# Kernel optimization log

Hardware: AMD Instinct MI355X
Metric: run time of the kernel (lower is better)

Reference implementation:

```python
import jax, jax.numpy as jnp
import numpy as np

N_NODES = 100000

def _sage_conv(x, edge_index, W_l, W_r, b):
    # PyG SAGEConv (aggr='mean'): out = lin_l(mean_{j in N(i)} x_j) + lin_r(x_i)
    src, dst = edge_index[0], edge_index[1]
    n = x.shape[0]
    agg = jax.ops.segment_sum(x[src], dst, num_segments=n)        # [N, F]
    deg = jax.ops.segment_sum(jnp.ones((src.shape[0],), x.dtype), dst, num_segments=n)
    mean = agg / jnp.maximum(deg, 1.0)[:, None]
    return mean @ W_l + b + x @ W_r

def setup_inputs() -> dict:
    key = jax.random.key(0)
    ks = jax.random.split(key, 8)
    d_in, d_hid, n_cls, n_edges = 64, 128, 40, 1000000
    x = jax.random.normal(ks[0], (N_NODES, d_in), dtype=jnp.float32)
    edge_index = jax.random.randint(ks[1], (2, n_edges), 0, N_NODES, dtype=jnp.int64)
    W1_l = jax.random.normal(ks[2], (d_in, d_hid), dtype=jnp.float32) * (1.0 / np.sqrt(d_in))
    W1_r = jax.random.normal(ks[3], (d_in, d_hid), dtype=jnp.float32) * (1.0 / np.sqrt(d_in))
    b1 = jnp.zeros((d_hid,), dtype=jnp.float32)
    W2_l = jax.random.normal(ks[4], (d_hid, n_cls), dtype=jnp.float32) * (1.0 / np.sqrt(d_hid))
    W2_r = jax.random.normal(ks[5], (d_hid, n_cls), dtype=jnp.float32) * (1.0 / np.sqrt(d_hid))
    b2 = jnp.zeros((n_cls,), dtype=jnp.float32)
    return {"x": x, "edge_index": edge_index, "W1_l": W1_l, "W1_r": W1_r, "b1": b1,
            "W2_l": W2_l, "W2_r": W2_r, "b2": b2}

def reference(x, edge_index, W1_l, W1_r, b1, W2_l, W2_r, b2):
    h = _sage_conv(x, edge_index, W1_l, W1_r, b1)
    h = jax.nn.relu(h)
    h = _sage_conv(h, edge_index, W2_l, W2_r, b2)
    return jax.nn.log_softmax(h, axis=1)
```

## Files before the change

kernel.cpp:

```cpp
#include <hip/hip_runtime.h>

#define N_NODES 100000
#define N_EDGES 1000000
#define D_IN    64
#define D_HID   128
#define N_CLS   40
#define PAD     48
#define NBUK    391
#define EB      512
#define EPB     1954
#define NCB     6250

typedef float f32x4 __attribute__((ext_vector_type(4)));
typedef float f32x2 __attribute__((ext_vector_type(2)));
typedef short s8v   __attribute__((ext_vector_type(8)));
typedef unsigned short us8 __attribute__((ext_vector_type(8)));

__device__ __forceinline__ unsigned short f2bf(float f) {
    unsigned int b = __float_as_uint(f);
    return (unsigned short)((b + 0x7FFFu + ((b >> 16) & 1u)) >> 16);
}
__device__ __forceinline__ float bf2f(unsigned short u) {
    return __uint_as_float(((unsigned int)u) << 16);
}

#if __has_builtin(__builtin_amdgcn_cvt_pk_f32_fp8) && __has_builtin(__builtin_amdgcn_cvt_pk_fp8_f32)
#define HWFP8 1
#else
#define HWFP8 0
#endif

__device__ __forceinline__ unsigned int f2fp8_sw(float f) {
    const unsigned int b = __float_as_uint(f);
    const float g = __uint_as_float(b & 0x7FFFFFFFu) * 0x1p-120f;
    const unsigned int gb = __float_as_uint(g);
    const unsigned int r = gb + 0x7FFFFu + ((gb >> 20) & 1u);
    return ((b >> 31) << 7) | ((r >> 20) & 0x7Fu);
}
__device__ __forceinline__ float fp82f_sw(unsigned int u) {
    const unsigned int bits = ((u & 0x80u) << 24) | ((u & 0x7Fu) << 20);
    return __uint_as_float(bits) * 0x1p120f;
}
__device__ __forceinline__ unsigned int enc4(float a, float b, float c, float d) {
#if HWFP8
    int v = __builtin_amdgcn_cvt_pk_fp8_f32(a, b, 0, false);
    v = __builtin_amdgcn_cvt_pk_fp8_f32(c, d, v, true);
    return (unsigned int)v;
#else
    return f2fp8_sw(a) | (f2fp8_sw(b) << 8) | (f2fp8_sw(c) << 16) | (f2fp8_sw(d) << 24);
#endif
}
__device__ __forceinline__ void dec8_acc2(uint2 u, f32x2* a2) {
#if HWFP8
    a2[0] += __builtin_amdgcn_cvt_pk_f32_fp8((int)u.x, false);
    a2[1] += __builtin_amdgcn_cvt_pk_f32_fp8((int)u.x, true);
    a2[2] += __builtin_amdgcn_cvt_pk_f32_fp8((int)u.y, false);
    a2[3] += __builtin_amdgcn_cvt_pk_f32_fp8((int)u.y, true);
#else
    a2[0][0] += fp82f_sw(u.x & 0xFFu);        a2[0][1] += fp82f_sw((u.x >> 8) & 0xFFu);
    a2[1][0] += fp82f_sw((u.x >> 16) & 0xFFu); a2[1][1] += fp82f_sw((u.x >> 24) & 0xFFu);
    a2[2][0] += fp82f_sw(u.y & 0xFFu);        a2[2][1] += fp82f_sw((u.y >> 8) & 0xFFu);
    a2[3][0] += fp82f_sw((u.y >> 16) & 0xFFu); a2[3][1] += fp82f_sw((u.y >> 24) & 0xFFu);
#endif
}

__global__ __launch_bounds__(256) void passA_kern(
    const int* __restrict__ dst, int* __restrict__ cnt,
    const float* __restrict__ x,
    unsigned short* __restrict__ xb, unsigned char* __restrict__ xq,
    const float* __restrict__ W1l, const float* __restrict__ W1r,
    const float* __restrict__ W2l, const float* __restrict__ W2r,
    unsigned short* __restrict__ w1f, unsigned short* __restrict__ w2f)
{
    __shared__ int lbuk[NBUK];
    const int t = threadIdx.x;
    const int bid = blockIdx.x;
    if (bid < EB) {
        for (int j = t; j < NBUK; j += 256) lbuk[j] = 0;
        __syncthreads();
        const int e0 = bid * EPB;
        const int e1 = min(e0 + EPB, N_EDGES);
        for (int e = e0 + t; e < e1; e += 256) atomicAdd(&lbuk[dst[e] >> 8], 1);
        __syncthreads();
        for (int j = t; j < NBUK; j += 256) cnt[j * EB + bid] = lbuk[j];
        return;
    }
    const int i = (bid - EB) * 256 + t;
    if (i < 2048) {
        const int fid = i >> 6, l = i & 63;
        const int ct = fid >> 2, ks = fid & 3;
        const int c = ct * 16 + (l & 15);
        const int k0 = ks * 32 + 8 * (l >> 4);
        unsigned short tmp[8];
        #pragma unroll
        for (int j = 0; j < 8; ++j) {
            const int k = k0 + j;
            const float v = (k < 64) ? W1l[k * D_HID + c] : W1r[(k - 64) * D_HID + c];
            tmp[j] = f2bf(v);
        }
        *(s8v*)(w1f + (size_t)fid * 512 + l * 8) = *(s8v*)tmp;
    } else if (i < 2048 + 1280) {
        const int t2 = i - 2048;
        const int fid = t2 >> 6, l = t2 & 63;
        const int c2t = fid >> 2, ks = fid & 3;
        const int c2 = c2t * 16 + (l & 15);
        const int k0 = ks * 32 + 8 * (l >> 4);
        unsigned short tmp[8];
        #pragma unroll
        for (int j = 0; j < 8; ++j) {
            const int k = k0 + j;
            const float v = (c2 < N_CLS) ? W2l[k * N_CLS + c2] : W2r[k * N_CLS + (c2 - N_CLS)];
            tmp[j] = f2bf(v);
        }
        *(s8v*)(w2f + (size_t)fid * 512 + l * 8) = *(s8v*)tmp;
    }
    if (i >= N_NODES * (D_IN / 4)) return;
    const float4 v = reinterpret_cast<const float4*>(x)[i];
    ushort4 o;
    o.x = f2bf(v.x); o.y = f2bf(v.y); o.z = f2bf(v.z); o.w = f2bf(v.w);
    reinterpret_cast<ushort4*>(xb)[i] = o;
    reinterpret_cast<unsigned int*>(xq)[i] = enc4(v.x, v.y, v.z, v.w);
}

__global__ __launch_bounds__(512) void scanS1_kern(int* __restrict__ cnt, int* __restrict__ buktot)
{
    __shared__ int wsum[8];
    __shared__ int woff[8];
    const int buk = blockIdx.x;
    const int t = threadIdx.x;
    const int lane = t & 63, wid = t >> 6;
    const int v = cnt[buk * EB + t];
    int vs = v;
    #pragma unroll
    for (int off = 1; off < 64; off <<= 1) {
        int tt = __shfl_up(vs, off);
        if (lane >= off) vs += tt;
    }
    if (lane == 63) wsum[wid] = vs;
    __syncthreads();
    if (wid == 0 && lane < 8) {
        int w = wsum[lane];
        int ws_ = w;
        #pragma unroll
        for (int off = 1; off < 8; off <<= 1) {
            int tt = __shfl_up(ws_, off);
            if (lane >= off) ws_ += tt;
        }
        woff[lane] = ws_ - w;
        if (lane == 7) buktot[buk] = ws_;
    }
    __syncthreads();
    cnt[buk * EB + t] = woff[wid] + vs - v;
}

__global__ __launch_bounds__(512) void scanS2_kern(const int* __restrict__ buktot, int* __restrict__ bukbase)
{
    __shared__ int wsum[8];
    __shared__ int woff[8];
    const int t = threadIdx.x;
    const int lane = t & 63, wid = t >> 6;
    const int v = (t < NBUK) ? buktot[t] : 0;
    int vs = v;
    #pragma unroll
    for (int off = 1; off < 64; off <<= 1) {
        int tt = __shfl_up(vs, off);
        if (lane >= off) vs += tt;
    }
    if (lane == 63) wsum[wid] = vs;
    __syncthreads();
    if (wid == 0 && lane < 8) {
        int w = wsum[lane];
        int ws_ = w;
        #pragma unroll
        for (int off = 1; off < 8; off <<= 1) {
            int tt = __shfl_up(ws_, off);
            if (lane >= off) ws_ += tt;
        }
        woff[lane] = ws_ - w;
    }
    __syncthreads();
    if (t < NBUK) bukbase[t] = woff[wid] + vs - v;
}

__global__ __launch_bounds__(256) void passA2_kern(
    const int* __restrict__ src, const int* __restrict__ dst,
    const int* __restrict__ cnt, const int* __restrict__ bukbase,
    unsigned int* __restrict__ ebuf)
{
    __shared__ int cur[NBUK];
    const int t = threadIdx.x;
    const int blk = blockIdx.x;
    for (int j = t; j < NBUK; j += 256) cur[j] = bukbase[j] + cnt[j * EB + blk];
    __syncthreads();
    const int e0 = blk * EPB;
    const int e1 = min(e0 + EPB, N_EDGES);
    for (int e = e0 + t; e < e1; e += 256) {
        const int d = dst[e];
        const int slot = atomicAdd(&cur[d >> 8], 1);
        ebuf[slot] = (unsigned int)src[e] | ((unsigned int)(d & 255) << 17);
    }
}

__global__ __launch_bounds__(256) void passB_kern(
    const unsigned int* __restrict__ ebuf,
    const int* __restrict__ bukbase, const int* __restrict__ buktot,
    int* __restrict__ padcsr, int* __restrict__ deg)
{
    __shared__ int lh[256];
    const int t = threadIdx.x;
    const int b = blockIdx.x;
    lh[t] = 0;
    __syncthreads();
    const int base = bukbase[b];
    const int n = buktot[b];
    for (int j = t; j < n; j += 256) {
        const unsigned int u = ebuf[base + j];
        const int dl = (int)(u >> 17);
        const int sr = (int)(u & 0x1FFFFu);
        const int r = atomicAdd(&lh[dl], 1);
        if (r < PAD) padcsr[((b << 8) | dl) * PAD + r] = sr;
    }
    __syncthreads();
    const int node = (b << 8) + t;
    if (node < N_NODES) deg[node] = lh[t];
}

#define MLD 72
__global__ __launch_bounds__(512) void fused_mfma_kern(
    const unsigned short* __restrict__ xb, const unsigned char* __restrict__ xq,
    const int* __restrict__ deg, const int* __restrict__ padcsr,
    const unsigned short* __restrict__ w1f, const unsigned short* __restrict__ w2f,
    const float* __restrict__ b1, const float* __restrict__ b2,
    unsigned char* __restrict__ y2q, unsigned short* __restrict__ yrb)
{
    __shared__ unsigned short hT[8192];
    __shared__ unsigned short mean_lds[64 * MLD];
    const int t = threadIdx.x;
    const int l = t & 63, w = t >> 6;

    {
        const int s = l >> 3, c8 = l & 7;
        const int nl = w * 8 + s;
        const int gnode = blockIdx.x * 64 + nl;
        f32x2 a2[4] = {}, b2v[4] = {};
        float a[8];
        if (gnode < N_NODES) {
            const int dg = deg[gnode];
            const int beg = gnode * PAD;
            const int end = beg + min(dg, PAD);
            int j = beg;
            for (; j + 4 <= end; j += 4) {
                const int s0 = padcsr[j], s1 = padcsr[j + 1], s2 = padcsr[j + 2], s3 = padcsr[j + 3];
                const uint2 u0 = *(const uint2*)(xq + (size_t)s0 * D_IN + c8 * 8);
                const uint2 u1 = *(const uint2*)(xq + (size_t)s1 * D_IN + c8 * 8);
                const uint2 u2 = *(const uint2*)(xq + (size_t)s2 * D_IN + c8 * 8);
                const uint2 u3 = *(const uint2*)(xq + (size_t)s3 * D_IN + c8 * 8);
                dec8_acc2(u0, a2); dec8_acc2(u1, b2v);
                dec8_acc2(u2, a2); dec8_acc2(u3, b2v);
            }
            for (; j < end; ++j) {
                const int s0 = padcsr[j];
                const uint2 u0 = *(const uint2*)(xq + (size_t)s0 * D_IN + c8 * 8);
                dec8_acc2(u0, a2);
            }
            const float invd = 1.0f / fmaxf((float)dg, 1.0f);
            #pragma unroll
            for (int i = 0; i < 4; ++i) {
                a2[i] += b2v[i];
                a[2 * i]     = a2[i][0] * invd;
                a[2 * i + 1] = a2[i][1] * invd;
            }
        } else {
            #pragma unroll
            for (int i = 0; i < 8; ++i) a[i] = 0.f;
        }
        us8 o;
        #pragma unroll
        for (int i = 0; i < 8; ++i) o[i] = f2bf(a[i]);
        *(us8*)(mean_lds + nl * MLD + c8 * 8) = o;
    }
    __syncthreads();

    const int nt = w & 3;
    const int cg = w >> 2;
    const int node = blockIdx.x * 64 + nt * 16 + (l & 15);
    const int kc = 8 * (l >> 4);

    const unsigned short* xrow = xb + (size_t)node * D_IN;
    const unsigned short* mbase = mean_lds + (nt * 16 + (l & 15)) * MLD;
    s8v bfr[4];
    bfr[0] = *(const s8v*)(mbase + kc);
    bfr[1] = *(const s8v*)(mbase + 32 + kc);
    bfr[2] = *(const s8v*)(xrow + kc);
    bfr[3] = *(const s8v*)(xrow + 32 + kc);

    #pragma unroll
    for (int i = 0; i < 4; ++i) {
        const int ct = cg + 2 * i;
        f32x4 acc = {0.f, 0.f, 0.f, 0.f};
        #pragma unroll
        for (int ks = 0; ks < 4; ++ks) {
            const s8v a = *(const s8v*)(w1f + (size_t)(ct * 4 + ks) * 512 + l * 8);
            acc = __builtin_amdgcn_mfma_f32_16x16x32_bf16(a, bfr[ks], acc, 0, 0, 0);
        }
        const int c0 = 16 * ct + 4 * (l >> 4);
        const float4 bb = *reinterpret_cast<const float4*>(b1 + c0);
        const float h0 = fmaxf(acc[0] + bb.x, 0.f);
        const float h1 = fmaxf(acc[1] + bb.y, 0.f);
        const float h2 = fmaxf(acc[2] + bb.z, 0.f);
        const float h3 = fmaxf(acc[3] + bb.w, 0.f);
        uint2 pk;
        pk.x = (unsigned int)f2bf(h0) | ((unsigned int)f2bf(h1) << 16);
        pk.y = (unsigned int)f2bf(h2) | ((unsigned int)f2bf(h3) << 16);
        const int chunk = (nt * 4 + (c0 >> 5)) * 64 + (((c0 >> 3) & 3) << 4) + (l & 15);
        *reinterpret_cast<uint2*>(hT + chunk * 8 + (c0 & 7)) = pk;
    }
    __syncthreads();

    s8v hfr[4];
    #pragma unroll
    for (int ks = 0; ks < 4; ++ks)
        hfr[ks] = *(const s8v*)(hT + ((size_t)(nt * 4 + ks) * 64 + l) * 8);

    const int nc2 = (cg == 0) ? 3 : 2;
    const int c2t0 = (cg == 0) ? 0 : 3;
    for (int i = 0; i < nc2; ++i) {
        const int c2t = c2t0 + i;
        f32x4 acc = {0.f, 0.f, 0.f, 0.f};
        #pragma unroll
        for (int ks = 0; ks < 4; ++ks) {
            const s8v a = *(const s8v*)(w2f + (size_t)(c2t * 4 + ks) * 512 + l * 8);
            acc = __builtin_amdgcn_mfma_f32_16x16x32_bf16(a, hfr[ks], acc, 0, 0, 0);
        }
        const int c2 = c2t * 16 + 4 * (l >> 4);
        if (node < N_NODES) {
            if (c2 < N_CLS) {
                *reinterpret_cast<unsigned int*>(y2q + (size_t)node * N_CLS + c2) =
                    enc4(acc[0], acc[1], acc[2], acc[3]);
            } else {
                const int cr = c2 - N_CLS;
                const float4 bv = *reinterpret_cast<const float4*>(b2 + cr);
                uint2 pk;
                pk.x = (unsigned int)f2bf(acc[0] + bv.x) | ((unsigned int)f2bf(acc[1] + bv.y) << 16);
                pk.y = (unsigned int)f2bf(acc[2] + bv.z) | ((unsigned int)f2bf(acc[3] + bv.w) << 16);
                *reinterpret_cast<uint2*>(yrb + (size_t)node * N_CLS + cr) = pk;
            }
        }
    }
}

__global__ __launch_bounds__(256) void agg2final_kern(const unsigned char* __restrict__ y2q,
                                                      const int* __restrict__ deg,
                                                      const int* __restrict__ padcsr,
                                                      const unsigned short* __restrict__ yrb,
                                                      float* __restrict__ out)
{
    const int lane = threadIdx.x & 63;
    const int wid  = threadIdx.x >> 6;
    const int s = lane >> 3, c = lane & 7;
    const int node = blockIdx.x * 32 + wid * 8 + s;
    if (node >= N_NODES) return;
    const int dg = deg[node];
    const int beg = node * PAD;
    const int end = beg + min(dg, PAD);
    f32x2 a2[4] = {};
    if (c < 5) {
        for (int j = beg; j < end; ++j) {
            const int sn = padcsr[j];
            const uint2 u = *reinterpret_cast<const uint2*>(y2q + (size_t)sn * N_CLS + c * 8);
            dec8_acc2(u, a2);
        }
    }
    float l8[8];
    float m = -INFINITY;
    if (c < 5) {
        const float invd = 1.0f / fmaxf((float)dg, 1.0f);
        const us8 yv = *(const us8*)(yrb + (size_t)node * N_CLS + c * 8);
        #pragma unroll
        for (int i = 0; i < 8; ++i) {
            l8[i] = a2[i >> 1][i & 1] * invd + bf2f(yv[i]);
            m = fmaxf(m, l8[i]);
        }
    }
    #pragma unroll
    for (int off = 1; off < 8; off <<= 1) m = fmaxf(m, __shfl_xor(m, off));
    float sum = 0.f;
    if (c < 5) {
        #pragma unroll
        for (int i = 0; i < 8; ++i) sum += __expf(l8[i] - m);
    }
    #pragma unroll
    for (int off = 1; off < 8; off <<= 1) sum += __shfl_xor(sum, off);
    const float ls = m + __logf(sum);
    if (c < 5) {
        float4 o0 = {l8[0] - ls, l8[1] - ls, l8[2] - ls, l8[3] - ls};
        float4 o1 = {l8[4] - ls, l8[5] - ls, l8[6] - ls, l8[7] - ls};
        float* op = out + (size_t)node * N_CLS + c * 8;
        *reinterpret_cast<float4*>(op) = o0;
        *reinterpret_cast<float4*>(op + 4) = o1;
    }
}

extern "C" void kernel_launch(void* const* d_in, const int* in_sizes, int n_in,
                              void* d_out, int out_size, void* d_ws, size_t ws_size,
                              hipStream_t stream)
{
    const float* x   = (const float*)d_in[0];
    const int*   ei  = (const int*)  d_in[1];
    const float* W1l = (const float*)d_in[2];
    const float* W1r = (const float*)d_in[3];
    const float* b1  = (const float*)d_in[4];
    const float* W2l = (const float*)d_in[5];
    const float* W2r = (const float*)d_in[6];
    const float* b2  = (const float*)d_in[7];
    const int* src = ei;
    const int* dst = ei + N_EDGES;
    float* out = (float*)d_out;

    char* base = (char*)d_ws;
    int*            cnt     = (int*)           (base + 0);
    int*            buktot  = (int*)           (base + 800768);
    int*            bukbase = (int*)           (base + 802336);
    int*            deg     = (int*)           (base + 803904);
    unsigned int*   ebuf    = (unsigned int*)  (base + 1203904);
    int*            padcsr  = (int*)           (base + 5203904);
    unsigned short* xb      = (unsigned short*)(base + 24403904);
    unsigned char*  xq      = (unsigned char*) (base + 37208000);
    unsigned short* w1f     = (unsigned short*)(base + 43610048);
    unsigned short* w2f     = (unsigned short*)(base + 43642816);
    unsigned char*  y2q     = (unsigned char*) (base + 43663296);
    unsigned short* yrb     = (unsigned short*)(base + 47664576);

    passA_kern<<<EB + NCB, 256, 0, stream>>>(dst, cnt, x, xb, xq,
                                             W1l, W1r, W2l, W2r, w1f, w2f);
    scanS1_kern<<<NBUK, 512, 0, stream>>>(cnt, buktot);
    scanS2_kern<<<1, 512, 0, stream>>>(buktot, bukbase);
    passA2_kern<<<EB, 256, 0, stream>>>(src, dst, cnt, bukbase, ebuf);
    passB_kern<<<NBUK, 256, 0, stream>>>(ebuf, bukbase, buktot, padcsr, deg);

    fused_mfma_kern<<<(N_NODES + 63) / 64, 512, 0, stream>>>(
        xb, xq, deg, padcsr, w1f, w2f, b1, b2, y2q, yrb);
    agg2final_kern<<<(N_NODES + 31) / 32, 256, 0, stream>>>(
        y2q, deg, padcsr, yrb, out);
}
```

Measured before the change: 104.0 us.

## Stage CSR in LDS, widen fp8 gathers to 16 bytes, pad y2 rows

Both aggregation kernels now copy each block's padded CSR slice and degrees into shared memory before gathering. Neighbour rows are fetched with 16-byte fp8 loads instead of 8-byte ones: in layer 1, two half-wave groups split the edges and are combined with a shuffle; in layer 2, y2q and yrb rows are padded to 48 entries so each node uses 3 lanes instead of 5. The edge-bucketing pass also switches to fewer, larger blocks (256 instead of 512), and the scan and workspace offsets are adjusted to match. In exchange the kernels use more LDS and the padded rows cost extra workspace and writes, including zeroing the y2q pad.

```diff
diff --git a/kernel.cpp b/kernel.cpp
--- a/kernel.cpp
+++ b/kernel.cpp
@@ -7,9 +7,11 @@
 #define N_CLS   40
 #define PAD     48
 #define NBUK    391
-#define EB      512
-#define EPB     1954
+#define EB      256
+#define EPB     3907
 #define NCB     6250
+#define Y2LD    48
+#define YRLD    48
 
 typedef float f32x4 __attribute__((ext_vector_type(4)));
 typedef float f32x2 __attribute__((ext_vector_type(2)));
@@ -50,17 +52,25 @@
     return f2fp8_sw(a) | (f2fp8_sw(b) << 8) | (f2fp8_sw(c) << 16) | (f2fp8_sw(d) << 24);
 #endif
 }
-__device__ __forceinline__ void dec8_acc2(uint2 u, f32x2* a2) {
+__device__ __forceinline__ void dec16_acc(uint4 u, f32x2* a2) {
 #if HWFP8
     a2[0] += __builtin_amdgcn_cvt_pk_f32_fp8((int)u.x, false);
     a2[1] += __builtin_amdgcn_cvt_pk_f32_fp8((int)u.x, true);
     a2[2] += __builtin_amdgcn_cvt_pk_f32_fp8((int)u.y, false);
     a2[3] += __builtin_amdgcn_cvt_pk_f32_fp8((int)u.y, true);
+    a2[4] += __builtin_amdgcn_cvt_pk_f32_fp8((int)u.z, false);
+    a2[5] += __builtin_amdgcn_cvt_pk_f32_fp8((int)u.z, true);
+    a2[6] += __builtin_amdgcn_cvt_pk_f32_fp8((int)u.w, false);
+    a2[7] += __builtin_amdgcn_cvt_pk_f32_fp8((int)u.w, true);
 #else
-    a2[0][0] += fp82f_sw(u.x & 0xFFu);        a2[0][1] += fp82f_sw((u.x >> 8) & 0xFFu);
+    a2[0][0] += fp82f_sw(u.x & 0xFFu);         a2[0][1] += fp82f_sw((u.x >> 8) & 0xFFu);
     a2[1][0] += fp82f_sw((u.x >> 16) & 0xFFu); a2[1][1] += fp82f_sw((u.x >> 24) & 0xFFu);
-    a2[2][0] += fp82f_sw(u.y & 0xFFu);        a2[2][1] += fp82f_sw((u.y >> 8) & 0xFFu);
+    a2[2][0] += fp82f_sw(u.y & 0xFFu);         a2[2][1] += fp82f_sw((u.y >> 8) & 0xFFu);
     a2[3][0] += fp82f_sw((u.y >> 16) & 0xFFu); a2[3][1] += fp82f_sw((u.y >> 24) & 0xFFu);
+    a2[4][0] += fp82f_sw(u.z & 0xFFu);         a2[4][1] += fp82f_sw((u.z >> 8) & 0xFFu);
+    a2[5][0] += fp82f_sw((u.z >> 16) & 0xFFu); a2[5][1] += fp82f_sw((u.z >> 24) & 0xFFu);
+    a2[6][0] += fp82f_sw(u.w & 0xFFu);         a2[6][1] += fp82f_sw((u.w >> 8) & 0xFFu);
+    a2[7][0] += fp82f_sw((u.w >> 16) & 0xFFu); a2[7][1] += fp82f_sw((u.w >> 24) & 0xFFu);
 #endif
 }
 
@@ -122,10 +132,10 @@
     reinterpret_cast<unsigned int*>(xq)[i] = enc4(v.x, v.y, v.z, v.w);
 }
 
-__global__ __launch_bounds__(512) void scanS1_kern(int* __restrict__ cnt, int* __restrict__ buktot)
-{
-    __shared__ int wsum[8];
-    __shared__ int woff[8];
+__global__ __launch_bounds__(256) void scanS1_kern(int* __restrict__ cnt, int* __restrict__ buktot)
+{
+    __shared__ int wsum[4];
+    __shared__ int woff[4];
     const int buk = blockIdx.x;
     const int t = threadIdx.x;
     const int lane = t & 63, wid = t >> 6;
@@ -138,16 +148,16 @@
     }
     if (lane == 63) wsum[wid] = vs;
     __syncthreads();
-    if (wid == 0 && lane < 8) {
+    if (wid == 0 && lane < 4) {
         int w = wsum[lane];
         int ws_ = w;
         #pragma unroll
-        for (int off = 1; off < 8; off <<= 1) {
+        for (int off = 1; off < 4; off <<= 1) {
             int tt = __shfl_up(ws_, off);
             if (lane >= off) ws_ += tt;
         }
         woff[lane] = ws_ - w;
-        if (lane == 7) buktot[buk] = ws_;
+        if (lane == 3) buktot[buk] = ws_;
     }
     __syncthreads();
     cnt[buk * EB + t] = woff[wid] + vs - v;
@@ -235,49 +245,57 @@
 {
     __shared__ unsigned short hT[8192];
     __shared__ unsigned short mean_lds[64 * MLD];
+    __shared__ int csr_lds[64 * PAD];
+    __shared__ int deg_lds[64];
     const int t = threadIdx.x;
     const int l = t & 63, w = t >> 6;
+
+    {
+        const uint4* pc = (const uint4*)(padcsr + (size_t)blockIdx.x * 64 * PAD);
+        uint4* cl = (uint4*)csr_lds;
+        for (int i = t; i < 64 * PAD / 4; i += 512) cl[i] = pc[i];
+        if (t < 64) {
+            const int gn = blockIdx.x * 64 + t;
+            deg_lds[t] = (gn < N_NODES) ? min(deg[gn], PAD) : 0;
+        }
+    }
+    __syncthreads();
 
     {
         const int s = l >> 3, c8 = l & 7;
         const int nl = w * 8 + s;
-        const int gnode = blockIdx.x * 64 + nl;
-        f32x2 a2[4] = {}, b2v[4] = {};
-        float a[8];
-        if (gnode < N_NODES) {
-            const int dg = deg[gnode];
-            const int beg = gnode * PAD;
-            const int end = beg + min(dg, PAD);
-            int j = beg;
-            for (; j + 4 <= end; j += 4) {
-                const int s0 = padcsr[j], s1 = padcsr[j + 1], s2 = padcsr[j + 2], s3 = padcsr[j + 3];
-                const uint2 u0 = *(const uint2*)(xq + (size_t)s0 * D_IN + c8 * 8);
-                const uint2 u1 = *(const uint2*)(xq + (size_t)s1 * D_IN + c8 * 8);
-                const uint2 u2 = *(const uint2*)(xq + (size_t)s2 * D_IN + c8 * 8);
-                const uint2 u3 = *(const uint2*)(xq + (size_t)s3 * D_IN + c8 * 8);
-                dec8_acc2(u0, a2); dec8_acc2(u1, b2v);
-                dec8_acc2(u2, a2); dec8_acc2(u3, b2v);
-            }
-            for (; j < end; ++j) {
-                const int s0 = padcsr[j];
-                const uint2 u0 = *(const uint2*)(xq + (size_t)s0 * D_IN + c8 * 8);
-                dec8_acc2(u0, a2);
-            }
+        const int half = c8 >> 2, q = c8 & 3;
+        f32x2 a2[8] = {}, b2v[8] = {};
+        const int dg = deg_lds[nl];
+        const int* myidx = csr_lds + nl * PAD;
+        int j = half;
+        for (; j + 2 < dg; j += 4) {
+            const int s0 = myidx[j], s1 = myidx[j + 2];
+            const uint4 u0 = *(const uint4*)(xq + (size_t)s0 * D_IN + q * 16);
+            const uint4 u1 = *(const uint4*)(xq + (size_t)s1 * D_IN + q * 16);
+            dec16_acc(u0, a2);
+            dec16_acc(u1, b2v);
+        }
+        for (; j < dg; j += 2) {
+            const int s0 = myidx[j];
+            const uint4 u0 = *(const uint4*)(xq + (size_t)s0 * D_IN + q * 16);
+            dec16_acc(u0, a2);
+        }
+        #pragma unroll
+        for (int i = 0; i < 8; ++i) a2[i] += b2v[i];
+        #pragma unroll
+        for (int i = 0; i < 8; ++i) {
+            a2[i][0] += __shfl_xor(a2[i][0], 4);
+            a2[i][1] += __shfl_xor(a2[i][1], 4);
+        }
+        if (c8 < 4) {
             const float invd = 1.0f / fmaxf((float)dg, 1.0f);
+            unsigned short o[16];
             #pragma unroll
-            for (int i = 0; i < 4; ++i) {
-                a2[i] += b2v[i];
-                a[2 * i]     = a2[i][0] * invd;
-                a[2 * i + 1] = a2[i][1] * invd;
-            }
-        } else {
-            #pragma unroll
-            for (int i = 0; i < 8; ++i) a[i] = 0.f;
-        }
-        us8 o;
-        #pragma unroll
-        for (int i = 0; i < 8; ++i) o[i] = f2bf(a[i]);
-        *(us8*)(mean_lds + nl * MLD + c8 * 8) = o;
+            for (int i = 0; i < 16; ++i) o[i] = f2bf(a2[i >> 1][i & 1] * invd);
+            *(us8*)(mean_lds + nl * MLD + q * 16)     = *(us8*)o;
+            *(us8*)(mean_lds + nl * MLD + q * 16 + 8) = *(us8*)(o + 8);
+        }
     }
     __syncthreads();
 
@@ -335,7 +353,7 @@
         const int c2 = c2t * 16 + 4 * (l >> 4);
         if (node < N_NODES) {
             if (c2 < N_CLS) {
-                *reinterpret_cast<unsigned int*>(y2q + (size_t)node * N_CLS + c2) =
+                *reinterpret_cast<unsigned int*>(y2q + (size_t)node * Y2LD + c2) =
                     enc4(acc[0], acc[1], acc[2], acc[3]);
             } else {
                 const int cr = c2 - N_CLS;
@@ -343,7 +361,9 @@
                 uint2 pk;
                 pk.x = (unsigned int)f2bf(acc[0] + bv.x) | ((unsigned int)f2bf(acc[1] + bv.y) << 16);
                 pk.y = (unsigned int)f2bf(acc[2] + bv.z) | ((unsigned int)f2bf(acc[3] + bv.w) << 16);
-                *reinterpret_cast<uint2*>(yrb + (size_t)node * N_CLS + cr) = pk;
+                *reinterpret_cast<uint2*>(yrb + (size_t)node * YRLD + cr) = pk;
+                if (c2t == 2)
+                    *reinterpret_cast<unsigned int*>(y2q + (size_t)node * Y2LD + c2) = 0u;
             }
         }
     }
@@ -355,49 +375,80 @@
                                                       const unsigned short* __restrict__ yrb,
                                                       float* __restrict__ out)
 {
-    const int lane = threadIdx.x & 63;
-    const int wid  = threadIdx.x >> 6;
-    const int s = lane >> 3, c = lane & 7;
-    const int node = blockIdx.x * 32 + wid * 8 + s;
-    if (node >= N_NODES) return;
-    const int dg = deg[node];
-    const int beg = node * PAD;
-    const int end = beg + min(dg, PAD);
-    f32x2 a2[4] = {};
-    if (c < 5) {
-        for (int j = beg; j < end; ++j) {
-            const int sn = padcsr[j];
-            const uint2 u = *reinterpret_cast<const uint2*>(y2q + (size_t)sn * N_CLS + c * 8);
-            dec8_acc2(u, a2);
-        }
-    }
-    float l8[8];
+    __shared__ int csr_lds[64 * PAD];
+    __shared__ int deg_lds[64];
+    const int t = threadIdx.x;
+    const int lane = t & 63, wid = t >> 6;
+    {
+        const uint4* pc = (const uint4*)(padcsr + (size_t)blockIdx.x * 64 * PAD);
+        uint4* cl = (uint4*)csr_lds;
+        for (int i = t; i < 64 * PAD / 4; i += 256) cl[i] = pc[i];
+        if (t < 64) {
+            const int gn = blockIdx.x * 64 + t;
+            deg_lds[t] = (gn < N_NODES) ? min(deg[gn], PAD) : 0;
+        }
+    }
+    __syncthreads();
+
+    const int s = lane >> 2, c4 = lane & 3;
+    const int nl = wid * 16 + s;
+    const int node = blockIdx.x * 64 + nl;
+    const int dg = deg_lds[nl];
+    const bool act = (node < N_NODES) && (c4 < 3);
+    f32x2 a2[8] = {}, b2v[8] = {};
+    if (act) {
+        const int* myidx = csr_lds + nl * PAD;
+        int j = 0;
+        for (; j + 1 < dg; j += 2) {
+            const int s0 = myidx[j], s1 = myidx[j + 1];
+            const uint4 u0 = *(const uint4*)(y2q + (size_t)s0 * Y2LD + c4 * 16);
+            const uint4 u1 = *(const uint4*)(y2q + (size_t)s1 * Y2LD + c4 * 16);
+            dec16_acc(u0, a2);
+            dec16_acc(u1, b2v);
+        }
+        if (j < dg) {
+            const int s0 = myidx[j];
+            const uint4 u0 = *(const uint4*)(y2q + (size_t)s0 * Y2LD + c4 * 16);
+            dec16_acc(u0, a2);
+        }
+        #pragma unroll
+        for (int i = 0; i < 8; ++i) a2[i] += b2v[i];
+    }
+    float l16[16];
     float m = -INFINITY;
-    if (c < 5) {
+    if (act) {
         const float invd = 1.0f / fmaxf((float)dg, 1.0f);
-        const us8 yv = *(const us8*)(yrb + (size_t)node * N_CLS + c * 8);
-        #pragma unroll
-        for (int i = 0; i < 8; ++i) {
-            l8[i] = a2[i >> 1][i & 1] * invd + bf2f(yv[i]);
-            m = fmaxf(m, l8[i]);
-        }
-    }
-    #pragma unroll
-    for (int off = 1; off < 8; off <<= 1) m = fmaxf(m, __shfl_xor(m, off));
+        const us8 yv0 = *(const us8*)(yrb + (size_t)node * YRLD + c4 * 16);
+        const us8 yv1 = *(const us8*)(yrb + (size_t)node * YRLD + c4 * 16 + 8);
+        #pragma unroll
+        for (int i = 0; i < 16; ++i) {
+            const unsigned short yw = (i < 8) ? yv0[i] : yv1[i - 8];
+            const float v = a2[i >> 1][i & 1] * invd + bf2f(yw);
+            l16[i] = (c4 * 16 + i < N_CLS) ? v : -INFINITY;
+            m = fmaxf(m, l16[i]);
+        }
+    }
+    #pragma unroll
+    for (int off = 1; off < 4; off <<= 1) m = fmaxf(m, __shfl_xor(m, off));
     float sum = 0.f;
-    if (c < 5) {
-        #pragma unroll
-        for (int i = 0; i < 8; ++i) sum += __expf(l8[i] - m);
-    }
-    #pragma unroll
-    for (int off = 1; off < 8; off <<= 1) sum += __shfl_xor(sum, off);
+    if (act) {
+        #pragma unroll
+        for (int i = 0; i < 16; ++i) sum += __expf(l16[i] - m);
+    }
+    #pragma unroll
+    for (int off = 1; off < 4; off <<= 1) sum += __shfl_xor(sum, off);
     const float ls = m + __logf(sum);
-    if (c < 5) {
-        float4 o0 = {l8[0] - ls, l8[1] - ls, l8[2] - ls, l8[3] - ls};
-        float4 o1 = {l8[4] - ls, l8[5] - ls, l8[6] - ls, l8[7] - ls};
-        float* op = out + (size_t)node * N_CLS + c * 8;
-        *reinterpret_cast<float4*>(op) = o0;
-        *reinterpret_cast<float4*>(op + 4) = o1;
+    if (act) {
+        float* op = out + (size_t)node * N_CLS + c4 * 16;
+        const int nf4 = (c4 == 2) ? 2 : 4;
+        #pragma unroll
+        for (int i4 = 0; i4 < 4; ++i4) {
+            if (i4 < nf4) {
+                float4 o = {l16[i4 * 4] - ls, l16[i4 * 4 + 1] - ls,
+                            l16[i4 * 4 + 2] - ls, l16[i4 * 4 + 3] - ls};
+                *reinterpret_cast<float4*>(op + i4 * 4) = o;
+            }
+        }
     }
 }
 
@@ -419,27 +470,27 @@
 
     char* base = (char*)d_ws;
     int*            cnt     = (int*)           (base + 0);
-    int*            buktot  = (int*)           (base + 800768);
-    int*            bukbase = (int*)           (base + 802336);
-    int*            deg     = (int*)           (base + 803904);
-    unsigned int*   ebuf    = (unsigned int*)  (base + 1203904);
-    int*            padcsr  = (int*)           (base + 5203904);
-    unsigned short* xb      = (unsigned short*)(base + 24403904);
-    unsigned char*  xq      = (unsigned char*) (base + 37208000);
-    unsigned short* w1f     = (unsigned short*)(base + 43610048);
-    unsigned short* w2f     = (unsigned short*)(base + 43642816);
-    unsigned char*  y2q     = (unsigned char*) (base + 43663296);
-    unsigned short* yrb     = (unsigned short*)(base + 47664576);
+    int*            buktot  = (int*)           (base + 400384);
+    int*            bukbase = (int*)           (base + 401952);
+    int*            deg     = (int*)           (base + 403520);
+    unsigned int*   ebuf    = (unsigned int*)  (base + 803520);
+    int*            padcsr  = (int*)           (base + 4803520);
+    unsigned short* xb      = (unsigned short*)(base + 24009664);
+    unsigned char*  xq      = (unsigned char*) (base + 36813760);
+    unsigned short* w1f     = (unsigned short*)(base + 43215808);
+    unsigned short* w2f     = (unsigned short*)(base + 43248576);
+    unsigned char*  y2q     = (unsigned char*) (base + 43269056);
+    unsigned short* yrb     = (unsigned short*)(base + 48070592);
 
     passA_kern<<<EB + NCB, 256, 0, stream>>>(dst, cnt, x, xb, xq,
                                              W1l, W1r, W2l, W2r, w1f, w2f);
-    scanS1_kern<<<NBUK, 512, 0, stream>>>(cnt, buktot);
+    scanS1_kern<<<NBUK, 256, 0, stream>>>(cnt, buktot);
     scanS2_kern<<<1, 512, 0, stream>>>(buktot, bukbase);
     passA2_kern<<<EB, 256, 0, stream>>>(src, dst, cnt, bukbase, ebuf);
     passB_kern<<<NBUK, 256, 0, stream>>>(ebuf, bukbase, buktot, padcsr, deg);
 
     fused_mfma_kern<<<(N_NODES + 63) / 64, 512, 0, stream>>>(
         xb, xq, deg, padcsr, w1f, w2f, b1, b2, y2q, yrb);
-    agg2final_kern<<<(N_NODES + 31) / 32, 256, 0, stream>>>(
+    agg2final_kern<<<(N_NODES + 63) / 64, 256, 0, stream>>>(
         y2q, deg, padcsr, yrb, out);
 }
```

Result: faster. 98.47 us (-5.3%).
